# Performance work log

Measured on AMD Instinct MI355X. Metric: run time of the kernel, lower is better.

The kernel has to match this reference:

```python
import math
import jax, jax.numpy as jnp
import numpy as np

B, NPC, K, D, T, L = 512, 32, 12, 64, 64, 4  # crystals, atoms/crystal, knn, node_dim, time_dim, layers
N = B * NPC
E_IN = 2 * D + 1 + T   # 193
N_IN = 2 * D + T       # 192


def setup_inputs() -> dict:
    key = jax.random.key(0)
    ks = jax.random.split(key, 32)
    rn = lambda k, shp, s=0.05: jax.random.normal(k, shp, jnp.float32) * s
    inp = {}
    inp["z_nodes"] = jax.random.normal(ks[0], (N, 128), jnp.float32)
    inp["t"] = jax.random.uniform(ks[1], (B,), jnp.float32) * 1000.0
    inp["frac_coords"] = jax.random.uniform(ks[2], (N, 3), jnp.float32)
    inp["lattice"] = jnp.eye(3, dtype=jnp.float32) * 5.0 + rn(ks[3], (B, 3, 3), 0.3)
    inp["batch_indices"] = jnp.repeat(jnp.arange(B, dtype=jnp.int32), NPC)
    inp["num_atoms"] = NPC
    # time_mlp: Linear(T, 2T) -> SiLU -> Linear(2T, T)
    inp["time_w1"] = rn(ks[4], (T, 2 * T)); inp["time_b1"] = rn(ks[5], (2 * T,))
    inp["time_w2"] = rn(ks[6], (2 * T, T)); inp["time_b2"] = rn(ks[7], (T,))
    # node_embedding: Linear(128, D)
    inp["emb_w"] = rn(ks[8], (128, D)); inp["emb_b"] = rn(ks[9], (D,))
    # per-layer EGNN params stacked on leading L axis
    inp["edge_w1"] = rn(ks[10], (L, E_IN, D)); inp["edge_b1"] = rn(ks[11], (L, D))
    inp["edge_w2"] = rn(ks[12], (L, D, D));    inp["edge_b2"] = rn(ks[13], (L, D))
    inp["coord_w1"] = rn(ks[14], (L, D, D));   inp["coord_b1"] = rn(ks[15], (L, D))
    inp["coord_w2"] = rn(ks[16], (L, D, 1))
    inp["node_w1"] = rn(ks[17], (L, N_IN, D)); inp["node_b1"] = rn(ks[18], (L, D))
    inp["node_w2"] = rn(ks[19], (L, D, D));    inp["node_b2"] = rn(ks[20], (L, D))
    return inp


def _forward(z_nodes, t, frac_coords, lattice, batch_indices, num_atoms,
             time_w1, time_b1, time_w2, time_b2, emb_w, emb_b,
             edge_w1, edge_b1, edge_w2, edge_b2, coord_w1, coord_b1, coord_w2,
             node_w1, node_b1, node_w2, node_b2):
    silu = jax.nn.silu
    n = num_atoms
    b = lattice.shape[0]
    n_nodes = z_nodes.shape[0]

    # ---- time embedding ----
    half = T // 2
    freqs = jnp.exp(jnp.arange(half, dtype=jnp.float32) * (-math.log(10000.0) / (half - 1)))
    ang = t[:, None] * freqs[None, :]
    sinu = jnp.concatenate([jnp.sin(ang), jnp.cos(ang)], axis=-1)  # [B, T]
    t_feat = silu(sinu @ time_w1 + time_b1) @ time_w2 + time_b2     # [B, T]
    t_nodes = t_feat[batch_indices]                                  # [N, T]

    h = z_nodes @ emb_w + emb_b                                      # [N, D]

    # ---- vectorized PBC KNN graph (all crystals have n atoms) ----
    f = frac_coords.reshape(b, n, 3)
    diff_f = f[:, :, None, :] - f[:, None, :, :]
    diff_f = diff_f - jnp.round(diff_f)
    diff_c = jnp.einsum('bijk,bkl->bijl', diff_f, lattice)           # [b,n,n,3]
    dist_sq = jnp.sum(diff_c * diff_c, axis=-1)                      # [b,n,n]
    dist_sq = jnp.where(jnp.eye(n, dtype=bool)[None], jnp.inf, dist_sq)
    k = min(K, n - 1)
    _, idx = jax.lax.top_k(-dist_sq, k)                              # [b,n,k] neighbor indices
    offs = (jnp.arange(b, dtype=jnp.int32) * n)[:, None, None]
    edge_src = (idx + offs).reshape(-1)                              # neighbors j
    edge_dst = (jnp.broadcast_to(jnp.arange(n, dtype=jnp.int32)[None, :, None], (b, n, k)) + offs).reshape(-1)
    diff_cart = jnp.take_along_axis(diff_c, jnp.broadcast_to(idx[..., None], (b, n, k, 3)), axis=2).reshape(-1, 3)
    dist_sq_e = jnp.take_along_axis(dist_sq, idx, axis=2).reshape(-1, 1)

    t_edges = t_nodes[edge_src]                                      # [E, T]

    total_shift = jnp.zeros((n_nodes, 3), dtype=h.dtype)
    for l in range(L):
        edge_in = jnp.concatenate([h[edge_src], h[edge_dst], dist_sq_e, t_edges], axis=-1)
        m = silu(edge_in @ edge_w1[l] + edge_b1[l])
        m = silu(m @ edge_w2[l] + edge_b2[l])                        # [E, D]
        cw = silu(m @ coord_w1[l] + coord_b1[l]) @ coord_w2[l]       # [E, 1]
        coord_update = jax.ops.segment_sum(diff_cart * cw, edge_src, num_segments=n_nodes)
        m_i = jax.ops.segment_sum(m, edge_dst, num_segments=n_nodes)
        node_in = jnp.concatenate([h, m_i, t_nodes], axis=-1)
        h = h + (silu(node_in @ node_w1[l] + node_b1[l]) @ node_w2[l] + node_b2[l])
        total_shift = total_shift + coord_update

    inv_lat = jnp.linalg.inv(lattice)[batch_indices]                 # [N,3,3]
    shift_frac = jnp.einsum('ni,nij->nj', total_shift, inv_lat)
    return shift_frac, h


def reference(z_nodes, t, frac_coords, lattice, batch_indices, num_atoms,
              time_w1, time_b1, time_w2, time_b2, emb_w, emb_b,
              edge_w1, edge_b1, edge_w2, edge_b2, coord_w1, coord_b1, coord_w2,
              node_w1, node_b1, node_w2, node_b2):
    return _forward(z_nodes, t, frac_coords, lattice, batch_indices, num_atoms,
                    time_w1, time_b1, time_w2, time_b2, emb_w, emb_b,
                    edge_w1, edge_b1, edge_w2, edge_b2, coord_w1, coord_b1, coord_w2,
                    node_w1, node_b1, node_w2, node_b2)
```

## Files before the change

kernel.cpp:

```cpp
#include <hip/hip_runtime.h>
#include <hip/hip_bf16.h>
#include <math.h>

#define NB 512
#define NPC 32
#define KNN 12
#define NL 4
#define NN (NB*NPC)
#define WPL 28672

typedef float v4f __attribute__((ext_vector_type(4)));
typedef float v2f __attribute__((ext_vector_type(2)));
typedef short s8v __attribute__((ext_vector_type(8)));

__device__ __forceinline__ float silu_f(float x) {
    return x * __builtin_amdgcn_rcpf(1.0f + __builtin_amdgcn_exp2f(x * -1.44269504088896341f));
}

__device__ __forceinline__ v2f silu2(v2f x) {
    v2f n = x * -1.44269504088896341f;
    v2f e; e.x = __builtin_amdgcn_exp2f(n.x); e.y = __builtin_amdgcn_exp2f(n.y);
    v2f d = e + 1.0f;
    v2f r; r.x = __builtin_amdgcn_rcpf(d.x); r.y = __builtin_amdgcn_rcpf(d.y);
    return x * r;
}

__device__ __forceinline__ unsigned short f2bf(float x) {
    unsigned u = __float_as_uint(x);
    u += 0x7fffu + ((u >> 16) & 1u);
    return (unsigned short)(u >> 16);
}

__device__ __forceinline__ unsigned pk2bf(float a, float b) {
    __hip_bfloat162 t = __float22bfloat162_rn(make_float2(a, b));
    union { __hip_bfloat162 h; unsigned u; } c; c.h = t;
    return c.u;
}
__device__ __forceinline__ unsigned pk2bfu(v2f s) { return pk2bf(s.x, s.y); }

__device__ __forceinline__ int div12(int e) { return (e * 1366) >> 14; }

template<int R>
__device__ __forceinline__ void gemm_acc(const float* A, int astride,
                                         const float* __restrict__ Wg,
                                         int K, int lane, float* acc) {
#pragma unroll 2
    for (int kq = 0; kq < (K >> 2); ++kq) {
        float w0 = Wg[(4*kq+0)*64 + lane];
        float w1 = Wg[(4*kq+1)*64 + lane];
        float w2 = Wg[(4*kq+2)*64 + lane];
        float w3 = Wg[(4*kq+3)*64 + lane];
#pragma unroll
        for (int r = 0; r < R; ++r) {
            float4 a = *(const float4*)(A + r*astride + 4*kq);
            acc[r] = fmaf(a.x, w0, acc[r]);
            acc[r] = fmaf(a.y, w1, acc[r]);
            acc[r] = fmaf(a.z, w2, acc[r]);
            acc[r] = fmaf(a.w, w3, acc[r]);
        }
    }
}

extern "C" __global__ void prepack_w(const float* __restrict__ edge_w1, const float* __restrict__ edge_w2,
                                     const float* __restrict__ coord_w1, const float* __restrict__ node_w1,
                                     const float* __restrict__ node_w2, unsigned short* __restrict__ wout) {
    int g = blockIdx.x * 256 + threadIdx.x;
    if (g >= 4 * WPL / 8) return;
    int l = (g * 8) / WPL;
    int r = (g * 8) % WPL;
    int base, nKt, mat;
    if      (r < 8192)  { base = 0;     nKt = 2; mat = 0; }
    else if (r < 12288) { base = 8192;  nKt = 2; mat = 1; }
    else if (r < 16384) { base = 12288; nKt = 2; mat = 2; }
    else if (r < 24576) { base = 16384; nKt = 4; mat = 3; }
    else                { base = 24576; nKt = 2; mat = 4; }
    int idx = r - base;
    int lane = (idx >> 3) & 63, t = idx >> 9;
    int kt = t % nKt, nt = t / nKt;
    int k0 = kt*32 + ((lane >> 4) & 3)*8;
    int n  = nt*16 + (lane & 15);
    unsigned short o[8];
#pragma unroll
    for (int j = 0; j < 8; ++j) {
        int k = k0 + j;
        float v;
        if      (mat == 0) v = (n < 64) ? edge_w1[l*193*64 + k*64 + n] : edge_w1[l*193*64 + (64+k)*64 + (n-64)];
        else if (mat == 1) v = edge_w2 [l*4096 + k*64 + n];
        else if (mat == 2) v = coord_w1[l*4096 + k*64 + n];
        else if (mat == 3) v = node_w1 [l*192*64 + k*64 + n];
        else               v = node_w2 [l*4096 + k*64 + n];
        o[j] = f2bf(v);
    }
    *(s8v*)(wout + g*8) = *(s8v*)o;
}

extern "C" __global__ __launch_bounds__(256, 2)
void crystal_fused(const float* __restrict__ z_nodes, const float* __restrict__ t_in,
                   const float* __restrict__ frac,    const float* __restrict__ lattice,
                   const float* __restrict__ time_w1, const float* __restrict__ time_b1,
                   const float* __restrict__ time_w2, const float* __restrict__ time_b2,
                   const float* __restrict__ emb_w,   const float* __restrict__ emb_b,
                   const float* __restrict__ edge_w1, const float* __restrict__ edge_b1,
                   const float* __restrict__ edge_b2, const float* __restrict__ coord_b1,
                   const float* __restrict__ coord_w2,
                   const float* __restrict__ node_w1, const float* __restrict__ node_b1,
                   const float* __restrict__ node_b2,
                   const unsigned short* __restrict__ wbf,
                   float* __restrict__ out)
{
    __shared__ __align__(16) float s_h[32*65];
    __shared__ __align__(16) unsigned short s_habf[32*136];
    __shared__ __align__(16) unsigned short s_n1bf[32*72];
    __shared__ __align__(16) float s_hs[32*68];
    __shared__ __align__(16) float s_hd[32*68];
    __shared__ __align__(16) unsigned short s_tiles16[9216];
    __shared__ float2 s_emeta[384];
    __shared__ float s_endc[384*3];
    __shared__ float s_frac[32][3];
    __shared__ float s_lat[9], s_inv[9];
    __shared__ float s_sinu[64], s_t1[128], s_tf[64];
    __shared__ float s_tb4[NL*64], s_nb4[NL*64];
    __shared__ float s_shift4[4*96];
    __shared__ float s_shift[96];
    __shared__ float s_w1r[64];

    float* dcf = (float*)s_tiles16;
    float (*s_dsq)[33] = (float(*)[33])s_n1bf;

    const int tid  = threadIdx.x;
    const int c    = blockIdx.x;
    const int lane = tid & 63;
    const int wave = tid >> 6;
    const int q4   = lane >> 4;
    const int c16  = lane & 15;
    const int base = c * NPC;

    if (tid < 96) {
        ((float*)s_frac)[tid] = frac[base*3 + tid];
    } else if (tid < 105) {
        s_lat[tid-96] = lattice[c*9 + (tid-96)];
    } else if (tid >= 128 && tid < 160) {
        int i = tid - 128;
        float freq = expf((float)i * (-9.210340371976184f / 31.0f));
        float ang  = t_in[c] * freq;
        s_sinu[i]    = sinf(ang);
        s_sinu[i+32] = cosf(ang);
    }
    __syncthreads();

    {
        float l00=s_lat[0],l01=s_lat[1],l02=s_lat[2];
        float l10=s_lat[3],l11=s_lat[4],l12=s_lat[5];
        float l20=s_lat[6],l21=s_lat[7],l22=s_lat[8];
        for (int p = tid; p < 1024; p += 256) {
            int i = p >> 5, j = p & 31;
            float dx = s_frac[i][0]-s_frac[j][0];
            float dy = s_frac[i][1]-s_frac[j][1];
            float dz = s_frac[i][2]-s_frac[j][2];
            dx -= rintf(dx); dy -= rintf(dy); dz -= rintf(dz);
            float cx = dx*l00 + dy*l10 + dz*l20;
            float cy = dx*l01 + dy*l11 + dz*l21;
            float cz = dx*l02 + dy*l12 + dz*l22;
            float dd = cx*cx + cy*cy + cz*cz;
            s_dsq[i][j] = (i==j) ? 3.0e38f : dd;
            dcf[p*3+0]=cx; dcf[p*3+1]=cy; dcf[p*3+2]=cz;
        }
    }
    __syncthreads();

    if (tid < 128) {
        int i = tid >> 2, g = tid & 3;
        float dl0 = s_dsq[i][g*8+0], dl1 = s_dsq[i][g*8+1];
        float dl2 = s_dsq[i][g*8+2], dl3 = s_dsq[i][g*8+3];
        float dl4 = s_dsq[i][g*8+4], dl5 = s_dsq[i][g*8+5];
        float dl6 = s_dsq[i][g*8+6], dl7 = s_dsq[i][g*8+7];
        for (int k = 0; k < KNN; ++k) {
            float v = dl0; int jl = g*8;
            if (dl1 < v) { v = dl1; jl = g*8+1; }
            if (dl2 < v) { v = dl2; jl = g*8+2; }
            if (dl3 < v) { v = dl3; jl = g*8+3; }
            if (dl4 < v) { v = dl4; jl = g*8+4; }
            if (dl5 < v) { v = dl5; jl = g*8+5; }
            if (dl6 < v) { v = dl6; jl = g*8+6; }
            if (dl7 < v) { v = dl7; jl = g*8+7; }
            float ov; int oj;
            ov = __shfl_xor(v, 1); oj = __shfl_xor(jl, 1);
            if (ov < v || (ov == v && oj < jl)) { v = ov; jl = oj; }
            ov = __shfl_xor(v, 2); oj = __shfl_xor(jl, 2);
            if (ov < v || (ov == v && oj < jl)) { v = ov; jl = oj; }
            if ((jl >> 3) == g) {
                int s = jl & 7;
                if      (s == 0) dl0 = 3.9e38f;
                else if (s == 1) dl1 = 3.9e38f;
                else if (s == 2) dl2 = 3.9e38f;
                else if (s == 3) dl3 = 3.9e38f;
                else if (s == 4) dl4 = 3.9e38f;
                else if (s == 5) dl5 = 3.9e38f;
                else if (s == 6) dl6 = 3.9e38f;
                else             dl7 = 3.9e38f;
            }
            if (g == 0) {
                int e = i*KNN + k;
                s_emeta[e] = make_float2(v, __int_as_float(jl));
                int p = (i<<5) + jl;
                s_endc[e*3+0] = dcf[p*3+0];
                s_endc[e*3+1] = dcf[p*3+1];
                s_endc[e*3+2] = dcf[p*3+2];
            }
        }
    } else {
        int jj = tid - 128;
        float p0 = time_b1[jj], p1=0.f, p2=0.f, p3=0.f;
        for (int k = 0; k < 64; k += 4) {
            p0 = fmaf(s_sinu[k+0], time_w1[(k+0)*128+jj], p0);
            p1 = fmaf(s_sinu[k+1], time_w1[(k+1)*128+jj], p1);
            p2 = fmaf(s_sinu[k+2], time_w1[(k+2)*128+jj], p2);
            p3 = fmaf(s_sinu[k+3], time_w1[(k+3)*128+jj], p3);
        }
        s_t1[jj] = silu_f((p0+p1) + (p2+p3));
    }
    __syncthreads();

    if (tid < 64) {
        float p0=time_b2[tid],p1=0.f,p2=0.f,p3=0.f;
        for (int k = 0; k < 128; k += 4) {
            p0 = fmaf(s_t1[k+0], time_w2[(k+0)*64+tid], p0);
            p1 = fmaf(s_t1[k+1], time_w2[(k+1)*64+tid], p1);
            p2 = fmaf(s_t1[k+2], time_w2[(k+2)*64+tid], p2);
            p3 = fmaf(s_t1[k+3], time_w2[(k+3)*64+tid], p3);
        }
        s_tf[tid] = (p0+p1) + (p2+p3);
    } else {
        for (int q = tid - 64; q < 384; q += 192) s_shift4[q] = 0.0f;
    }
    __syncthreads();

    float* zbuf = (float*)s_tiles16;
    for (int q = tid; q < 4096; q += 256) zbuf[q] = z_nodes[base*128 + q];
#pragma unroll
    for (int it = 0; it < 2; ++it) {
        int t = wave + it*4;
        int lt = t >> 1, kind = t & 1;
        const float* Wt = kind ? (node_w1 + lt*192*64 + 128*64) : (edge_w1 + lt*193*64 + 129*64);
        const float* bb = kind ? (node_b1 + lt*64) : (edge_b1 + lt*64);
        float p0 = bb[lane], p1=0.f, p2=0.f, p3=0.f;
        for (int k = 0; k < 64; k += 4) {
            p0 = fmaf(s_tf[k+0], Wt[(k+0)*64 + lane], p0);
            p1 = fmaf(s_tf[k+1], Wt[(k+1)*64 + lane], p1);
            p2 = fmaf(s_tf[k+2], Wt[(k+2)*64 + lane], p2);
            p3 = fmaf(s_tf[k+3], Wt[(k+3)*64 + lane], p3);
        }
        float v = (p0+p1) + (p2+p3);
        if (kind) s_nb4[lt*64 + lane] = v;
        else      s_tb4[lt*64 + lane] = v;
    }
    __syncthreads();

    {
        float acc[8];
#pragma unroll
        for (int r = 0; r < 8; ++r) acc[r] = emb_b[lane];
        gemm_acc<8>(zbuf + (wave*8)*128, 128, emb_w, 128, lane, acc);
#pragma unroll
        for (int r = 0; r < 8; ++r) {
            int row = wave*8 + r;
            s_h[row*65 + lane] = acc[r];
            s_habf[row*136 + lane] = f2bf(acc[r]);
        }
    }
    __syncthreads();

    for (int l = 0; l < NL; ++l) {
        const unsigned short* wl = wbf + l*WPL;

        if (tid < 64) s_w1r[tid] = edge_w1[l*193*64 + 128*64 + tid];

        float b2e_v[4], cb1_v[4], w2c_v[4];
#pragma unroll
        for (int nt = 0; nt < 4; ++nt) {
            b2e_v[nt] = edge_b2 [l*64 + nt*16 + c16];
            cb1_v[nt] = coord_b1[l*64 + nt*16 + c16];
            w2c_v[nt] = coord_w2[l*64 + nt*16 + c16];
        }

        s8v w2f[8], wc1f[8];
#pragma unroll
        for (int nt = 0; nt < 4; ++nt)
#pragma unroll
            for (int kt = 0; kt < 2; ++kt) {
                w2f [nt*2+kt] = *(const s8v*)(wl +  8192 + ((nt*2+kt)*64 + lane)*8);
                wc1f[nt*2+kt] = *(const s8v*)(wl + 12288 + ((nt*2+kt)*64 + lane)*8);
            }

        {
            s8v a[2][2];
#pragma unroll
            for (int mt = 0; mt < 2; ++mt)
#pragma unroll
                for (int kt = 0; kt < 2; ++kt)
                    a[mt][kt] = *(const s8v*)(s_habf + (mt*16 + c16)*136 + kt*32 + q4*8);
            v4f accS[2] = {{0.f,0.f,0.f,0.f},{0.f,0.f,0.f,0.f}};
            v4f accD[2] = {{0.f,0.f,0.f,0.f},{0.f,0.f,0.f,0.f}};
#pragma unroll
            for (int kt = 0; kt < 2; ++kt) {
                s8v bS = *(const s8v*)(wl + ((wave*2+kt)*64 + lane)*8);
                s8v bD = *(const s8v*)(wl + (((wave+4)*2+kt)*64 + lane)*8);
#pragma unroll
                for (int mt = 0; mt < 2; ++mt) {
                    accS[mt] = __builtin_amdgcn_mfma_f32_16x16x32_bf16(a[mt][kt], bS, accS[mt], 0, 0, 0);
                    accD[mt] = __builtin_amdgcn_mfma_f32_16x16x32_bf16(a[mt][kt], bD, accD[mt], 0, 0, 0);
                }
            }
            int col = wave*16 + c16;
            float tbv = s_tb4[l*64 + col];
#pragma unroll
            for (int mt = 0; mt < 2; ++mt)
#pragma unroll
                for (int reg = 0; reg < 4; ++reg) {
                    int row = mt*16 + q4*4 + reg;
                    s_hs[row*68 + col] = accS[mt][reg];
                    s_hd[row*68 + col] = accD[mt][reg] + tbv;
                }
        }
        __syncthreads();

        {
            unsigned short* tbase = s_tiles16 + wave*2304;
            float* myshift = s_shift4 + wave*96;
            float miacc[4][2];
#pragma unroll
            for (int a2 = 0; a2 < 4; ++a2) { miacc[a2][0] = 0.f; miacc[a2][1] = 0.f; }

            auto flushd = [&](int d) {
                int s = d & 1;
#pragma unroll
                for (int nt = 0; nt < 4; ++nt) {
                    float v = miacc[nt][s];
                    v += __shfl_xor(v, 16);
                    v += __shfl_xor(v, 32);
                    s_habf[(wave*8 + d)*136 + 64 + nt*16 + c16] = f2bf(v);
                    miacc[nt][s] = 0.f;
                }
            };

            float2 me0 = s_emeta[wave*96 +  0 + c16];
            float2 me1 = s_emeta[wave*96 + 16 + c16];
            float2 me2 = s_emeta[wave*96 + 32 + c16];
            float2 me3 = s_emeta[wave*96 + 48 + c16];
            float2 me4 = s_emeta[wave*96 + 64 + c16];
            float2 me5 = s_emeta[wave*96 + 80 + c16];

            union S8 { s8v v; unsigned u[4]; } A0, A1;
            {
                int srcn = __float_as_int(me0.y);
                int dstn = div12(wave*96 + c16);
                const float* hsr = s_hs + srcn*68;
                const float* hdr = s_hd + dstn*68;
                const float dq = me0.x;
#pragma unroll
                for (int g2 = 0; g2 < 4; ++g2) {
                    int off = ((g2 & 2) ? 32 : 0) + ((g2 & 1) ? 4 : 0) + q4*8;
                    float4 Hv = *(const float4*)(hsr + off);
                    float4 Gv = *(const float4*)(hdr + off);
                    float4 Wv = *(const float4*)(s_w1r + off);
                    v2f t0 = {Hv.x + Gv.x + Wv.x*dq, Hv.y + Gv.y + Wv.y*dq};
                    v2f t1 = {Hv.z + Gv.z + Wv.z*dq, Hv.w + Gv.w + Wv.w*dq};
                    unsigned lo  = pk2bfu(silu2(t0));
                    unsigned hi2 = pk2bfu(silu2(t1));
                    if (g2 < 2) { A0.u[g2*2] = lo; A0.u[g2*2+1] = hi2; }
                    else        { A1.u[(g2-2)*2] = lo; A1.u[(g2-2)*2+1] = hi2; }
                }
            }

#pragma unroll
            for (int m = 0; m < 6; ++m) {
                const int e0g = wave*96 + m*16;
                unsigned short* tile = tbase + (m & 1)*1152;

                const int dlo = (m < 3) ? m : m + 1;
                const int thr = 3 - (m % 3);
                const int slo = dlo & 1;
#pragma unroll
                for (int nt = 0; nt < 4; ++nt) {
                    v4f acc = {0.f,0.f,0.f,0.f};
                    acc = __builtin_amdgcn_mfma_f32_16x16x32_bf16(A0.v, w2f[nt*2+0], acc, 0,0,0);
                    acc = __builtin_amdgcn_mfma_f32_16x16x32_bf16(A1.v, w2f[nt*2+1], acc, 0,0,0);
                    int col = nt*16 + c16;
                    v2f z01 = {acc[0] + b2e_v[nt], acc[1] + b2e_v[nt]};
                    v2f z23 = {acc[2] + b2e_v[nt], acc[3] + b2e_v[nt]};
                    v2f s01 = silu2(z01), s23 = silu2(z23);
                    unsigned p01 = pk2bfu(s01), p23 = pk2bfu(s23);
                    tile[(q4*4 + 0)*72 + col] = (unsigned short)p01;
                    tile[(q4*4 + 1)*72 + col] = (unsigned short)(p01 >> 16);
                    tile[(q4*4 + 2)*72 + col] = (unsigned short)p23;
                    tile[(q4*4 + 3)*72 + col] = (unsigned short)(p23 >> 16);
                    float msum = (s01.x + s01.y) + (s23.x + s23.y);
                    bool hi = (q4 >= thr);
                    miacc[nt][slo]     += hi ? 0.f : msum;
                    miacc[nt][slo ^ 1] += hi ? msum : 0.f;
                }

                if (m < 5) {
                    float2 men = (m==0) ? me1 : (m==1) ? me2 : (m==2) ? me3
                               : (m==3) ? me4 : me5;
                    int srcn = __float_as_int(men.y);
                    int dstn = div12(e0g + 16 + c16);
                    const float* hsr = s_hs + srcn*68;
                    const float* hdr = s_hd + dstn*68;
                    const float dqn = men.x;
#pragma unroll
                    for (int g2 = 0; g2 < 4; ++g2) {
                        int off = ((g2 & 2) ? 32 : 0) + ((g2 & 1) ? 4 : 0) + q4*8;
                        float4 Hv = *(const float4*)(hsr + off);
                        float4 Gv = *(const float4*)(hdr + off);
                        float4 Wv = *(const float4*)(s_w1r + off);
                        v2f t0 = {Hv.x + Gv.x + Wv.x*dqn, Hv.y + Gv.y + Wv.y*dqn};
                        v2f t1 = {Hv.z + Gv.z + Wv.z*dqn, Hv.w + Gv.w + Wv.w*dqn};
                        unsigned lo  = pk2bfu(silu2(t0));
                        unsigned hi2 = pk2bfu(silu2(t1));
                        if (g2 < 2) { A0.u[g2*2] = lo; A0.u[g2*2+1] = hi2; }
                        else        { A1.u[(g2-2)*2] = lo; A1.u[(g2-2)*2+1] = hi2; }
                    }
                }

                asm volatile("s_waitcnt lgkmcnt(0)" ::: "memory");
                s8v c0 = *(const s8v*)(tile + c16*72 +      q4*8);
                s8v c1 = *(const s8v*)(tile + c16*72 + 32 + q4*8);
                v2f cwp01 = {0.f, 0.f}, cwp23 = {0.f, 0.f};
#pragma unroll
                for (int nt = 0; nt < 4; ++nt) {
                    v4f acc = {0.f,0.f,0.f,0.f};
                    acc = __builtin_amdgcn_mfma_f32_16x16x32_bf16(c0, wc1f[nt*2+0], acc, 0,0,0);
                    acc = __builtin_amdgcn_mfma_f32_16x16x32_bf16(c1, wc1f[nt*2+1], acc, 0,0,0);
                    v2f z01 = {acc[0] + cb1_v[nt], acc[1] + cb1_v[nt]};
                    v2f z23 = {acc[2] + cb1_v[nt], acc[3] + cb1_v[nt]};
                    cwp01 += silu2(z01) * w2c_v[nt];
                    cwp23 += silu2(z23) * w2c_v[nt];
                }
                float cwp[4] = {cwp01.x, cwp01.y, cwp23.x, cwp23.y};
#pragma unroll
                for (int reg = 0; reg < 4; ++reg) {
                    float v = cwp[reg];
                    v += __shfl_xor(v, 1); v += __shfl_xor(v, 2);
                    v += __shfl_xor(v, 4); v += __shfl_xor(v, 8);
                    int e = e0g + q4*4 + reg;
                    if (c16 < 3) {
                        int src = __float_as_int(s_emeta[e].y);
                        atomicAdd(&myshift[src*3 + c16], s_endc[e*3 + c16] * v);
                    }
                }
                if (m == 0) { flushd(0); }
                else if (m == 1) { flushd(1); }
                else if (m == 2) { flushd(2); flushd(3); }
                else if (m == 3) { flushd(4); }
                else if (m == 4) { flushd(5); }
                else             { flushd(6); flushd(7); }
            }
        }

        const int mtA = wave & 1, nt0 = wave >> 1, nt1 = (wave >> 1) + 2;
        s8v bn1[8];
#pragma unroll
        for (int kt = 0; kt < 4; ++kt) {
            bn1[kt]   = *(const s8v*)(wl + 16384 + ((nt0*4+kt)*64 + lane)*8);
            bn1[4+kt] = *(const s8v*)(wl + 16384 + ((nt1*4+kt)*64 + lane)*8);
        }
        __syncthreads();

        {
            s8v aA[4];
#pragma unroll
            for (int kt = 0; kt < 4; ++kt)
                aA[kt] = *(const s8v*)(s_habf + (mtA*16 + c16)*136 + kt*32 + q4*8);
#pragma unroll
            for (int it = 0; it < 2; ++it) {
                int nt = it ? nt1 : nt0;
                int col = nt*16 + c16;
                float nbc = s_nb4[l*64 + col];
                v4f acc = {0.f,0.f,0.f,0.f};
#pragma unroll
                for (int kt = 0; kt < 4; ++kt)
                    acc = __builtin_amdgcn_mfma_f32_16x16x32_bf16(aA[kt], bn1[it*4+kt], acc, 0,0,0);
                v2f z01 = {acc[0] + nbc, acc[1] + nbc};
                v2f z23 = {acc[2] + nbc, acc[3] + nbc};
                unsigned p01 = pk2bfu(silu2(z01)), p23 = pk2bfu(silu2(z23));
                int r0 = mtA*16 + q4*4;
                s_n1bf[(r0+0)*72 + col] = (unsigned short)p01;
                s_n1bf[(r0+1)*72 + col] = (unsigned short)(p01 >> 16);
                s_n1bf[(r0+2)*72 + col] = (unsigned short)p23;
                s_n1bf[(r0+3)*72 + col] = (unsigned short)(p23 >> 16);
            }
        }
        s8v bn2[4];
        bn2[0] = *(const s8v*)(wl + 24576 + ((nt0*2+0)*64 + lane)*8);
        bn2[1] = *(const s8v*)(wl + 24576 + ((nt0*2+1)*64 + lane)*8);
        bn2[2] = *(const s8v*)(wl + 24576 + ((nt1*2+0)*64 + lane)*8);
        bn2[3] = *(const s8v*)(wl + 24576 + ((nt1*2+1)*64 + lane)*8);
        __syncthreads();

        {
            s8v a0 = *(const s8v*)(s_n1bf + (mtA*16 + c16)*72 +      q4*8);
            s8v a1 = *(const s8v*)(s_n1bf + (mtA*16 + c16)*72 + 32 + q4*8);
#pragma unroll
            for (int it = 0; it < 2; ++it) {
                int nt = it ? nt1 : nt0;
                int col = nt*16 + c16;
                float nb2_v = node_b2[l*64 + col];
                v4f acc = {0.f,0.f,0.f,0.f};
                acc = __builtin_amdgcn_mfma_f32_16x16x32_bf16(a0, bn2[it*2+0], acc, 0,0,0);
                acc = __builtin_amdgcn_mfma_f32_16x16x32_bf16(a1, bn2[it*2+1], acc, 0,0,0);
#pragma unroll
                for (int reg = 0; reg < 4; ++reg) {
                    int row = mtA*16 + q4*4 + reg;
                    float hn = s_h[row*65 + col] + acc[reg] + nb2_v;
                    s_h[row*65 + col] = hn;
                    s_habf[row*136 + col] = f2bf(hn);
                }
            }
        }
        __syncthreads();
    }

    if (tid == 0) {
        float a=s_lat[0],b=s_lat[1],cc=s_lat[2];
        float d=s_lat[3],e=s_lat[4],f =s_lat[5];
        float g=s_lat[6],h2=s_lat[7],i2=s_lat[8];
        float A  =  (e*i2 - f*h2);
        float Bm = -(d*i2 - f*g);
        float C  =  (d*h2 - e*g);
        float det = a*A + b*Bm + cc*C;
        float rd = 1.0f/det;
        s_inv[0] = A*rd;
        s_inv[1] = -(b*i2 - cc*h2)*rd;
        s_inv[2] =  (b*f  - cc*e )*rd;
        s_inv[3] = Bm*rd;
        s_inv[4] =  (a*i2 - cc*g )*rd;
        s_inv[5] = -(a*f  - cc*d )*rd;
        s_inv[6] = C*rd;
        s_inv[7] = -(a*h2 - b*g  )*rd;
        s_inv[8] =  (a*e  - b*d  )*rd;
    }
    if (tid < 96) {
        s_shift[tid] = s_shift4[tid] + s_shift4[96 + tid]
                     + s_shift4[192 + tid] + s_shift4[288 + tid];
    }
    __syncthreads();
    if (tid < 96) {
        int r = tid/3, j = tid%3;
        float v = s_shift[r*3+0]*s_inv[0*3+j]
                + s_shift[r*3+1]*s_inv[1*3+j]
                + s_shift[r*3+2]*s_inv[2*3+j];
        out[(base + r)*3 + j] = v;
    }
    for (int q = tid; q < 2048; q += 256) {
        int row = q >> 6, colq = q & 63;
        out[NN*3 + base*64 + q] = s_h[row*65 + colq];
    }
}

extern "C" void kernel_launch(void* const* d_in, const int* in_sizes, int n_in,
                              void* d_out, int out_size, void* d_ws, size_t ws_size,
                              hipStream_t stream) {
    unsigned short* wbf = (unsigned short*)d_ws;
    prepack_w<<<(4*WPL/8 + 255)/256, 256, 0, stream>>>(
        (const float*)d_in[12], (const float*)d_in[14], (const float*)d_in[16],
        (const float*)d_in[19], (const float*)d_in[21], wbf);
    crystal_fused<<<NB, 256, 0, stream>>>(
        (const float*)d_in[0],  (const float*)d_in[1],  (const float*)d_in[2],  (const float*)d_in[3],
        (const float*)d_in[6],  (const float*)d_in[7],  (const float*)d_in[8],  (const float*)d_in[9],
        (const float*)d_in[10], (const float*)d_in[11],
        (const float*)d_in[12], (const float*)d_in[13], (const float*)d_in[15],
        (const float*)d_in[17], (const float*)d_in[18],
        (const float*)d_in[19], (const float*)d_in[20], (const float*)d_in[22],
        wbf, (float*)d_out);
}
```

Measured before the change: 204.4 us.

## Prefetch edge gather into registers and single-buffer the per-wave edge tile

```diff
diff --git a/kernel.cpp b/kernel.cpp
--- a/kernel.cpp
+++ b/kernel.cpp
@@ -113,7 +113,7 @@
     __shared__ __align__(16) unsigned short s_n1bf[32*72];
     __shared__ __align__(16) float s_hs[32*68];
     __shared__ __align__(16) float s_hd[32*68];
-    __shared__ __align__(16) unsigned short s_tiles16[9216];
+    __shared__ __align__(16) unsigned short s_tiles16[8192];
     __shared__ float2 s_emeta[384];
     __shared__ float s_endc[384*3];
     __shared__ float s_frac[32][3];
@@ -122,9 +122,7 @@
     __shared__ float s_tb4[NL*64], s_nb4[NL*64];
     __shared__ float s_shift4[4*96];
     __shared__ float s_shift[96];
-    __shared__ float s_w1r[64];
-
-    float* dcf = (float*)s_tiles16;
+
     float (*s_dsq)[33] = (float(*)[33])s_n1bf;
 
     const int tid  = threadIdx.x;
@@ -148,6 +146,7 @@
     }
     __syncthreads();
 
+    float* dcf = (float*)s_tiles16;
     {
         float l00=s_lat[0],l01=s_lat[1],l02=s_lat[2];
         float l10=s_lat[3],l11=s_lat[4],l12=s_lat[5];
@@ -272,9 +271,7 @@
 
     for (int l = 0; l < NL; ++l) {
         const unsigned short* wl = wbf + l*WPL;
-
-        if (tid < 64) s_w1r[tid] = edge_w1[l*193*64 + 128*64 + tid];
-
+        const float* w1row = edge_w1 + l*193*64 + 128*64;
         float b2e_v[4], cb1_v[4], w2c_v[4];
 #pragma unroll
         for (int nt = 0; nt < 4; ++nt) {
@@ -291,6 +288,12 @@
                 w2f [nt*2+kt] = *(const s8v*)(wl +  8192 + ((nt*2+kt)*64 + lane)*8);
                 wc1f[nt*2+kt] = *(const s8v*)(wl + 12288 + ((nt*2+kt)*64 + lane)*8);
             }
+        union F4 { float4 v; float f[4]; };
+        F4 W4[4];
+        W4[0].v = *(const float4*)(w1row + q4*8);
+        W4[1].v = *(const float4*)(w1row + q4*8 + 4);
+        W4[2].v = *(const float4*)(w1row + 32 + q4*8);
+        W4[3].v = *(const float4*)(w1row + 32 + q4*8 + 4);
 
         {
             s8v a[2][2];
@@ -325,7 +328,7 @@
         __syncthreads();
 
         {
-            unsigned short* tbase = s_tiles16 + wave*2304;
+            unsigned short* tile = s_tiles16 + wave*1152;
             float* myshift = s_shift4 + wave*96;
             float miacc[4][2];
 #pragma unroll
@@ -350,32 +353,48 @@
             float2 me4 = s_emeta[wave*96 + 64 + c16];
             float2 me5 = s_emeta[wave*96 + 80 + c16];
 
-            union S8 { s8v v; unsigned u[4]; } A0, A1;
+            F4 H[4], G[4];
             {
                 int srcn = __float_as_int(me0.y);
                 int dstn = div12(wave*96 + c16);
-                const float* hsr = s_hs + srcn*68;
-                const float* hdr = s_hd + dstn*68;
-                const float dq = me0.x;
+                const float* hsr = s_hs + srcn*68 + q4*8;
+                const float* hdr = s_hd + dstn*68 + q4*8;
+                H[0].v = *(const float4*)(hsr);      H[1].v = *(const float4*)(hsr+4);
+                H[2].v = *(const float4*)(hsr+32);   H[3].v = *(const float4*)(hsr+36);
+                G[0].v = *(const float4*)(hdr);      G[1].v = *(const float4*)(hdr+4);
+                G[2].v = *(const float4*)(hdr+32);   G[3].v = *(const float4*)(hdr+36);
+            }
+
+#pragma unroll
+            for (int m = 0; m < 6; ++m) {
+                const int e0g = wave*96 + m*16;
+                const float dq = (m==0) ? me0.x : (m==1) ? me1.x : (m==2) ? me2.x
+                               : (m==3) ? me3.x : (m==4) ? me4.x : me5.x;
+                union S8 { s8v v; unsigned u[4]; } A0, A1;
 #pragma unroll
                 for (int g2 = 0; g2 < 4; ++g2) {
-                    int off = ((g2 & 2) ? 32 : 0) + ((g2 & 1) ? 4 : 0) + q4*8;
-                    float4 Hv = *(const float4*)(hsr + off);
-                    float4 Gv = *(const float4*)(hdr + off);
-                    float4 Wv = *(const float4*)(s_w1r + off);
-                    v2f t0 = {Hv.x + Gv.x + Wv.x*dq, Hv.y + Gv.y + Wv.y*dq};
-                    v2f t1 = {Hv.z + Gv.z + Wv.z*dq, Hv.w + Gv.w + Wv.w*dq};
+                    v2f h0 = {H[g2].f[0], H[g2].f[1]}, h1 = {H[g2].f[2], H[g2].f[3]};
+                    v2f g0 = {G[g2].f[0], G[g2].f[1]}, g1 = {G[g2].f[2], G[g2].f[3]};
+                    v2f w0 = {W4[g2].f[0], W4[g2].f[1]}, w1 = {W4[g2].f[2], W4[g2].f[3]};
+                    v2f t0 = h0 + g0 + w0 * dq;
+                    v2f t1 = h1 + g1 + w1 * dq;
                     unsigned lo  = pk2bfu(silu2(t0));
                     unsigned hi2 = pk2bfu(silu2(t1));
                     if (g2 < 2) { A0.u[g2*2] = lo; A0.u[g2*2+1] = hi2; }
                     else        { A1.u[(g2-2)*2] = lo; A1.u[(g2-2)*2+1] = hi2; }
                 }
-            }
-
-#pragma unroll
-            for (int m = 0; m < 6; ++m) {
-                const int e0g = wave*96 + m*16;
-                unsigned short* tile = tbase + (m & 1)*1152;
+                if (m < 5) {
+                    float2 men = (m==0) ? me1 : (m==1) ? me2 : (m==2) ? me3
+                               : (m==3) ? me4 : me5;
+                    int srcn = __float_as_int(men.y);
+                    int dstn = div12(e0g + 16 + c16);
+                    const float* hsr = s_hs + srcn*68 + q4*8;
+                    const float* hdr = s_hd + dstn*68 + q4*8;
+                    H[0].v = *(const float4*)(hsr);      H[1].v = *(const float4*)(hsr+4);
+                    H[2].v = *(const float4*)(hsr+32);   H[3].v = *(const float4*)(hsr+36);
+                    G[0].v = *(const float4*)(hdr);      G[1].v = *(const float4*)(hdr+4);
+                    G[2].v = *(const float4*)(hdr+32);   G[3].v = *(const float4*)(hdr+36);
+                }
 
                 const int dlo = (m < 3) ? m : m + 1;
                 const int thr = 3 - (m % 3);
@@ -399,30 +418,6 @@
                     miacc[nt][slo]     += hi ? 0.f : msum;
                     miacc[nt][slo ^ 1] += hi ? msum : 0.f;
                 }
-
-                if (m < 5) {
-                    float2 men = (m==0) ? me1 : (m==1) ? me2 : (m==2) ? me3
-                               : (m==3) ? me4 : me5;
-                    int srcn = __float_as_int(men.y);
-                    int dstn = div12(e0g + 16 + c16);
-                    const float* hsr = s_hs + srcn*68;
-                    const float* hdr = s_hd + dstn*68;
-                    const float dqn = men.x;
-#pragma unroll
-                    for (int g2 = 0; g2 < 4; ++g2) {
-                        int off = ((g2 & 2) ? 32 : 0) + ((g2 & 1) ? 4 : 0) + q4*8;
-                        float4 Hv = *(const float4*)(hsr + off);
-                        float4 Gv = *(const float4*)(hdr + off);
-                        float4 Wv = *(const float4*)(s_w1r + off);
-                        v2f t0 = {Hv.x + Gv.x + Wv.x*dqn, Hv.y + Gv.y + Wv.y*dqn};
-                        v2f t1 = {Hv.z + Gv.z + Wv.z*dqn, Hv.w + Gv.w + Wv.w*dqn};
-                        unsigned lo  = pk2bfu(silu2(t0));
-                        unsigned hi2 = pk2bfu(silu2(t1));
-                        if (g2 < 2) { A0.u[g2*2] = lo; A0.u[g2*2+1] = hi2; }
-                        else        { A1.u[(g2-2)*2] = lo; A1.u[(g2-2)*2+1] = hi2; }
-                    }
-                }
-
                 asm volatile("s_waitcnt lgkmcnt(0)" ::: "memory");
                 s8v c0 = *(const s8v*)(tile + c16*72 +      q4*8);
                 s8v c1 = *(const s8v*)(tile + c16*72 + 32 + q4*8);
```

Result: no change. 201.0 us (-1.7%).
